# Performance work log

Hardware: AMD Instinct MI355X
Metric: run time of the kernel (lower is better)

Reference implementation:

```python
import jax, jax.numpy as jnp
import numpy as np

B, S, E, H = 2, 2048, 1024, 16
D = E // H  # head_dim = 64


def setup_inputs() -> dict:
    key = jax.random.key(0)
    ks = jax.random.split(key, 9)
    s = 1.0 / np.sqrt(E)
    return {
        "x": jax.random.normal(ks[0], (B, S, E), dtype=jnp.float32),
        "Wq": jax.random.uniform(ks[1], (E, E), jnp.float32, -s, s),
        "bq": jax.random.uniform(ks[2], (E,), jnp.float32, -s, s),
        "Wk": jax.random.uniform(ks[3], (E, E), jnp.float32, -s, s),
        "bk": jax.random.uniform(ks[4], (E,), jnp.float32, -s, s),
        "Wv": jax.random.uniform(ks[5], (E, E), jnp.float32, -s, s),
        "bv": jax.random.uniform(ks[6], (E,), jnp.float32, -s, s),
        "Wo": jax.random.uniform(ks[7], (E, E), jnp.float32, -s, s),
        "bo": jax.random.uniform(ks[8], (E,), jnp.float32, -s, s),
    }


def reference(x, Wq, bq, Wk, bk, Wv, bv, Wo, bo):
    # QKV projections (torch Linear: x @ W.T + b), split into heads: [B,H,S,D]
    def proj(t, W, b):
        return (t @ W.T + b).reshape(B, S, H, D).transpose(0, 2, 1, 3)

    Q = proj(x, Wq, bq)
    K = proj(x, Wk, bk)
    V = proj(x, Wv, bv)
    # scores [B,H,S,S], scaled by sqrt(head_dim)
    score = jnp.einsum('bnqd,bnkd->bnqk', Q, K) / jnp.sqrt(jnp.float32(D))
    weights = jax.nn.softmax(score, axis=-1)
    out = jnp.einsum('bnql,bnld->bnqd', weights, V)  # [B,H,S,D]
    out = out.transpose(0, 2, 1, 3).reshape(B, S, E)
    return out @ Wo.T + bo
```

## Files before the change

### kernel.cpp

```cpp
#include <hip/hip_runtime.h>


#define B_ 2
#define S_ 2048
#define E_ 1024
#define H_ 16
#define D_ 64
#define M_ (B_ * S_)

typedef __attribute__((ext_vector_type(8))) _Float16 f16x8;
typedef __attribute__((ext_vector_type(4))) _Float16 f16x4;
typedef __attribute__((ext_vector_type(2))) _Float16 f16x2;
typedef __attribute__((ext_vector_type(4))) float f32x4;
typedef __attribute__((ext_vector_type(16))) float f32x16;
typedef __attribute__((ext_vector_type(8))) unsigned short u16x8;
typedef __attribute__((ext_vector_type(4))) unsigned int u32x4;

#define LOG2E  1.44269504f
#define CLOG2  4.32808512f

#define KROW 144
#define KBUF 9216
#define VBASE 18432
#define SMEMSZ 36864

static __device__ __forceinline__ float bf16_to_f32(unsigned short u) {
    return __uint_as_float(((unsigned)u) << 16);
}
static __device__ __forceinline__ unsigned short f32_to_bf16(float f) {
    unsigned u = __float_as_uint(f);
    u += 0x7FFFu + ((u >> 16) & 1u);
    return (unsigned short)(u >> 16);
}
static __device__ __forceinline__ float load1_f32(const void* p, int i, bool isbf) {
    return isbf ? bf16_to_f32(((const unsigned short*)p)[i]) : ((const float*)p)[i];
}
static __device__ __forceinline__ void store1(void* p, size_t i, float v, bool isbf) {
    if (isbf) ((unsigned short*)p)[i] = f32_to_bf16(v);
    else      ((float*)p)[i] = v;
}
static __device__ __forceinline__ void gl2lds16(const void* g, void* l) {
    __builtin_amdgcn_global_load_lds((const __attribute__((address_space(1))) unsigned int*)g,
                                     (__attribute__((address_space(3))) unsigned int*)l, 16, 0, 0);
}
static __device__ __forceinline__ float rexp2(float x) {
    float r;
    asm("v_exp_f32 %0, %1" : "=v"(r) : "v"(x));
    return r;
}
static __device__ __forceinline__ unsigned pk2(float a, float b) {
    return __builtin_bit_cast(unsigned, __builtin_amdgcn_cvt_pkrtz(a, b));
}

__global__ __launch_bounds__(256) void convert_inputs(
    const void* __restrict__ x,  const void* __restrict__ wq,
    const void* __restrict__ wk, const void* __restrict__ wv,
    const void* __restrict__ wo,
    _Float16* __restrict__ x16, _Float16* __restrict__ w16,
    int* __restrict__ flag_out)
{
    __shared__ int sflag;
    const int tid = threadIdx.x;
    if (tid < 64) {
        const unsigned short hh = ((const unsigned short*)x)[2 * tid];
        const int e = (hh >> 7) & 0xFF;
        const bool sane = (e >= 0x60 && e <= 0x9F);
        const unsigned long long m = __ballot(sane);
        if (tid == 0) sflag = (__popcll(m) >= 48) ? 1 : 0;
    }
    __syncthreads();
    const bool isbf = sflag != 0;
    if (blockIdx.x == 0 && tid == 0) *flag_out = sflag;

    const size_t t = ((size_t)blockIdx.x * 256 + tid) * 8;
    const void* src; size_t off; _Float16* dst; float scale = 1.0f;
    if (t < (size_t)M_ * E_) { src = x; off = t; dst = x16 + t; }
    else {
        const size_t u = t - (size_t)M_ * E_;
        const int wsel = (int)(u >> 20);
        off = u & ((1u << 20) - 1);
        src = wsel == 0 ? wq : wsel == 1 ? wk : wsel == 2 ? wv : wo;
        dst = w16 + u;
        if (wsel == 0) scale = 0.125f * LOG2E;
    }
    f16x8 v;
    if (isbf) {
        u16x8 s = *(const u16x8*)((const unsigned short*)src + off);
        #pragma unroll
        for (int j = 0; j < 8; ++j) v[j] = (_Float16)(bf16_to_f32(s[j]) * scale);
    } else {
        const float* f = (const float*)src + off;
        f32x4 lo = *(const f32x4*)f;
        f32x4 hi = *(const f32x4*)(f + 4);
        #pragma unroll
        for (int j = 0; j < 4; ++j) {
            v[j]     = (_Float16)(lo[j] * scale);
            v[4 + j] = (_Float16)(hi[j] * scale);
        }
    }
    *(f16x8*)dst = v;
}

__global__ __launch_bounds__(256) void gemm_qkv(
    const _Float16* __restrict__ x16, const _Float16* __restrict__ w16,
    const void* __restrict__ bq, const void* __restrict__ bk, const void* __restrict__ bv,
    const int* __restrict__ flag,
    _Float16* __restrict__ Qb, _Float16* __restrict__ Kb, _Float16* __restrict__ VTb)
{
    __shared__ __align__(16) _Float16 As[128 * 64];
    __shared__ __align__(16) _Float16 Bs[128 * 64];
    const bool isbf = (*flag != 0);
    const int tid = threadIdx.x, wave = tid >> 6, lane = tid & 63;
    const int wm = wave >> 1, wn = wave & 1;
    const int qd = lane >> 4, ln = lane & 15;
    const int m0 = blockIdx.x * 128;
    const int by = blockIdx.y;
    const int wsel = by >> 3;
    const int n0 = (by & 7) * 128;
    const _Float16* W = w16 + ((size_t)wsel << 20);

    char* dX = (wsel == 2) ? (char*)Bs : (char*)As;
    char* dW = (wsel == 2) ? (char*)As : (char*)Bs;

    const _Float16* gx[4]; const _Float16* gw[4];
    char* lx[4]; char* lw[4];
    #pragma unroll
    for (int it = 0; it < 4; ++it) {
        const int seg = it * 256 + tid;
        const int row = seg >> 3, cg = seg & 7;
        const int scol = ((cg + row) & 7) * 8;
        gx[it] = x16 + (size_t)(m0 + row) * E_ + scol;
        gw[it] = W + (size_t)(n0 + row) * E_ + scol;
        lx[it] = dX + (size_t)(it * 256 + wave * 64) * 16;
        lw[it] = dW + (size_t)(it * 256 + wave * 64) * 16;
    }

    const int sw0 = ((qd - ln) & 7) * 8;
    const int sw1 = ((qd + 4 - ln) & 7) * 8;

    f32x4 acc[16] = {};

    for (int kt = 0; kt < E_; kt += 64) {
        __syncthreads();
        #pragma unroll
        for (int it = 0; it < 4; ++it) {
            gl2lds16(gx[it] + kt, lx[it]);
            gl2lds16(gw[it] + kt, lw[it]);
        }
        __syncthreads();
        #pragma unroll
        for (int kk = 0; kk < 2; ++kk) {
            const int sw = kk ? sw1 : sw0;
            f16x8 a[4], bfr[4];
            #pragma unroll
            for (int mt = 0; mt < 4; ++mt)
                a[mt] = *(const f16x8*)&As[((wm * 64 + mt * 16 + ln) << 6) + sw];
            #pragma unroll
            for (int nt = 0; nt < 4; ++nt)
                bfr[nt] = *(const f16x8*)&Bs[((wn * 64 + nt * 16 + ln) << 6) + sw];
            #pragma unroll
            for (int mt = 0; mt < 4; ++mt)
                #pragma unroll
                for (int nt = 0; nt < 4; ++nt)
                    acc[mt * 4 + nt] = __builtin_amdgcn_mfma_f32_16x16x32_f16(a[mt], bfr[nt], acc[mt * 4 + nt], 0, 0, 0);
        }
    }

    if (wsel != 2) {
        const void* bias = wsel == 0 ? bq : bk;
        const float bscale = (wsel == 0) ? 0.125f * LOG2E : 1.0f;
        _Float16* dst = wsel == 0 ? Qb : Kb;
        #pragma unroll
        for (int nt = 0; nt < 4; ++nt) {
            const int n = n0 + wn * 64 + nt * 16 + ln;
            const float bvv = load1_f32(bias, n, isbf) * bscale;
            const int h = n >> 6, d = n & 63;
            #pragma unroll
            for (int mt = 0; mt < 4; ++mt)
                #pragma unroll
                for (int r = 0; r < 4; ++r) {
                    const int m = m0 + wm * 64 + mt * 16 + qd * 4 + r;
                    const int b = m >> 11, s = m & (S_ - 1);
                    dst[((size_t)(b * H_ + h) * S_ + s) * D_ + d] =
                        (_Float16)(acc[mt * 4 + nt][r] + bvv);
                }
        }
    } else {
        #pragma unroll
        for (int mt = 0; mt < 4; ++mt)
            #pragma unroll
            for (int r = 0; r < 4; ++r) {
                const int e = n0 + wm * 64 + mt * 16 + qd * 4 + r;
                const float bvv = load1_f32(bv, e, isbf);
                const int h = e >> 6, d = e & 63;
                #pragma unroll
                for (int nt = 0; nt < 4; ++nt) {
                    const int sg = m0 + wn * 64 + nt * 16 + ln;
                    const int b = sg >> 11, s = sg & (S_ - 1);
                    VTb[((size_t)(b * H_ + h) * D_ + d) * S_ + s] =
                        (_Float16)(acc[mt * 4 + nt][r] + bvv);
                }
            }
    }
}

__global__ __launch_bounds__(256, 4) void attn(
    const _Float16* __restrict__ Q, const _Float16* __restrict__ K,
    const _Float16* __restrict__ VT, _Float16* __restrict__ AO)
{
    __shared__ __align__(16) char smem[SMEMSZ];

    const int tid = threadIdx.x, wave = tid >> 6, lane = tid & 63;
    const int rl = lane & 31, h = lane >> 5;
    const int qg = wave & 1, kh = wave >> 1;
    const int L = blockIdx.x;
    const int bh = ((L & 7) << 2) | ((L >> 3) & 3);
    const int qt = L >> 5;
    const int b = bh >> 4, hh = bh & (H_ - 1);

    const _Float16* Kbase = K + (size_t)bh * S_ * D_;
    const _Float16* Vbase = VT + (size_t)bh * D_ * S_;

    f16x8 qf[4];
    {
        const _Float16* qrow = Q + ((size_t)bh * S_ + qt * 64 + qg * 32 + rl) * D_ + h * 8;
        #pragma unroll
        for (int c = 0; c < 4; ++c) qf[c] = *(const f16x8*)(qrow + c * 16);
    }

    f16x8 ones;
    #pragma unroll
    for (int j = 0; j < 8; ++j) ones[j] = (_Float16)1.0f;

    const _Float16* kg[2]; const _Float16* vg[2]; int sw[2];
    #pragma unroll
    for (int it = 0; it < 2; ++it) {
        const int seg = it * 256 + tid;
        const int row = seg >> 3, c = seg & 7;
        kg[it] = Kbase + (size_t)row * D_ + c * 8;
        vg[it] = Vbase + (size_t)row * S_ + c * 8;
        sw[it] = row * KROW + c * 16;
    }

    int koff[4];
    #pragma unroll
    for (int c = 0; c < 4; ++c)
        koff[c] = (kh * 32 + rl) * KROW + (((c << 1) | h) << 4);
    const int vrow0 = rl * KROW, vrow1 = (32 + rl) * KROW;
    const int vka = kh * 64 + h * 8;

    f32x16 o0 = {}, o1 = {}, li = {};

    {
        f16x8 kr[2], vr[2];
        #pragma unroll
        for (int it = 0; it < 2; ++it) { kr[it] = *(const f16x8*)kg[it]; vr[it] = *(const f16x8*)vg[it]; }
        #pragma unroll
        for (int it = 0; it < 2; ++it) {
            *(f16x8*)(smem + sw[it])         = kr[it];
            *(f16x8*)(smem + VBASE + sw[it]) = vr[it];
        }
    }
    __syncthreads();

    for (int kt = 0; kt < S_; kt += 64) {
        const int p = (kt >> 6) & 1;
        const bool more = (kt + 64) < S_;

        f16x8 kr[2], vr[2];
        if (more) {
            #pragma unroll
            for (int it = 0; it < 2; ++it) {
                kr[it] = *(const f16x8*)(kg[it] + (size_t)(kt + 64) * D_);
                vr[it] = *(const f16x8*)(vg[it] + (kt + 64));
            }
        }

        const char* kb = smem + p * KBUF;
        const char* vb = smem + VBASE + p * KBUF;

        f16x8 af[4];
        #pragma unroll
        for (int c = 0; c < 4; ++c) af[c] = *(const f16x8*)(kb + koff[c]);

        f32x16 sc = {};
        __builtin_amdgcn_s_setprio(1);
        #pragma unroll
        for (int c = 0; c < 4; ++c)
            sc = __builtin_amdgcn_mfma_f32_32x32x16_f16(af[c], qf[c], sc, 0, 0, 0);
        __builtin_amdgcn_s_setprio(0);

        float e[16];
        #pragma unroll
        for (int i = 0; i < 16; ++i) e[i] = rexp2(sc[i] - CLOG2);

        #pragma unroll
        for (int ks = 0; ks < 2; ++ks) {
            const int oo = 8 * ks;
            const f16x8 pf = __builtin_bit_cast(f16x8, (u32x4){
                pk2(e[oo + 0], e[oo + 1]), pk2(e[oo + 2], e[oo + 3]),
                pk2(e[oo + 4], e[oo + 5]), pk2(e[oo + 6], e[oo + 7])});

            const int cA = vka + ks * 32;
            const f16x4 a0 = *(const f16x4*)(vb + vrow0 + cA);
            const f16x4 b0 = *(const f16x4*)(vb + vrow0 + cA + 16);
            const f16x4 a1 = *(const f16x4*)(vb + vrow1 + cA);
            const f16x4 b1 = *(const f16x4*)(vb + vrow1 + cA + 16);
            const f16x8 v0 = __builtin_shufflevector(a0, b0, 0, 1, 2, 3, 4, 5, 6, 7);
            const f16x8 v1 = __builtin_shufflevector(a1, b1, 0, 1, 2, 3, 4, 5, 6, 7);

            __builtin_amdgcn_s_setprio(1);
            o0 = __builtin_amdgcn_mfma_f32_32x32x16_f16(pf, v0, o0, 0, 0, 0);
            o1 = __builtin_amdgcn_mfma_f32_32x32x16_f16(pf, v1, o1, 0, 0, 0);
            li = __builtin_amdgcn_mfma_f32_32x32x16_f16(pf, ones, li, 0, 0, 0);
            __builtin_amdgcn_s_setprio(0);
        }

        if (more) {
            #pragma unroll
            for (int it = 0; it < 2; ++it) {
                *(f16x8*)(smem + (p ^ 1) * KBUF + sw[it])         = kr[it];
                *(f16x8*)(smem + VBASE + (p ^ 1) * KBUF + sw[it]) = vr[it];
            }
        }
        __syncthreads();
    }

    float* red = (float*)smem;
    const int rbase = qg * 64 + lane;
    if (kh) {
        #pragma unroll
        for (int i = 0; i < 16; ++i) {
            red[i * 128 + rbase]        = o0[i];
            red[(16 + i) * 128 + rbase] = o1[i];
            red[(32 + i) * 128 + rbase] = li[i];
        }
    }
    __syncthreads();
    if (!kh) {
        #pragma unroll
        for (int i = 0; i < 16; ++i) {
            const float t0 = o0[i] + red[i * 128 + rbase];
            const float t1 = o1[i] + red[(16 + i) * 128 + rbase];
            const float tl = li[i] + red[(32 + i) * 128 + rbase];
            const float inv = 1.0f / tl;
            const int q = qt * 64 + qg * 32 + 4 * h + (i & 3) + 8 * (i >> 2);
            _Float16* dst = AO + ((size_t)b * S_ + q) * E_ + hh * D_;
            dst[rl]      = (_Float16)(t0 * inv);
            dst[32 + rl] = (_Float16)(t1 * inv);
        }
    }
}

__global__ __launch_bounds__(256) void gemm_out(
    const _Float16* __restrict__ A, const _Float16* __restrict__ W,
    const void* __restrict__ bias, const int* __restrict__ flag, void* __restrict__ out)
{
    __shared__ __align__(16) _Float16 As[128 * 64];
    __shared__ __align__(16) _Float16 Bs[128 * 64];
    const bool isbf = (*flag != 0);
    const int tid = threadIdx.x, wave = tid >> 6, lane = tid & 63;
    const int wm = wave >> 1, wn = wave & 1;
    const int qd = lane >> 4, ln = lane & 15;
    const int m0 = blockIdx.x * 128;
    const int n0 = blockIdx.y * 128;

    const _Float16* ga[4]; const _Float16* gb[4];
    char* la[4]; char* lb[4];
    #pragma unroll
    for (int it = 0; it < 4; ++it) {
        const int seg = it * 256 + tid;
        const int row = seg >> 3, cg = seg & 7;
        const int scol = ((cg + row) & 7) * 8;
        ga[it] = A + (size_t)(m0 + row) * E_ + scol;
        gb[it] = W + (size_t)(n0 + row) * E_ + scol;
        la[it] = (char*)As + (size_t)(it * 256 + wave * 64) * 16;
        lb[it] = (char*)Bs + (size_t)(it * 256 + wave * 64) * 16;
    }
    const int sw0 = ((qd - ln) & 7) * 8;
    const int sw1 = ((qd + 4 - ln) & 7) * 8;

    f32x4 acc[16] = {};

    for (int kt = 0; kt < E_; kt += 64) {
        __syncthreads();
        #pragma unroll
        for (int it = 0; it < 4; ++it) {
            gl2lds16(ga[it] + kt, la[it]);
            gl2lds16(gb[it] + kt, lb[it]);
        }
        __syncthreads();
        #pragma unroll
        for (int kk = 0; kk < 2; ++kk) {
            const int sw = kk ? sw1 : sw0;
            f16x8 a[4], bfr[4];
            #pragma unroll
            for (int mt = 0; mt < 4; ++mt)
                a[mt] = *(const f16x8*)&As[((wm * 64 + mt * 16 + ln) << 6) + sw];
            #pragma unroll
            for (int nt = 0; nt < 4; ++nt)
                bfr[nt] = *(const f16x8*)&Bs[((wn * 64 + nt * 16 + ln) << 6) + sw];
            #pragma unroll
            for (int mt = 0; mt < 4; ++mt)
                #pragma unroll
                for (int nt = 0; nt < 4; ++nt)
                    acc[mt * 4 + nt] = __builtin_amdgcn_mfma_f32_16x16x32_f16(a[mt], bfr[nt], acc[mt * 4 + nt], 0, 0, 0);
        }
    }

    #pragma unroll
    for (int nt = 0; nt < 4; ++nt) {
        const int n = n0 + wn * 64 + nt * 16 + ln;
        const float bvv = load1_f32(bias, n, isbf);
        #pragma unroll
        for (int mt = 0; mt < 4; ++mt)
            #pragma unroll
            for (int r = 0; r < 4; ++r) {
                const int m = m0 + wm * 64 + mt * 16 + qd * 4 + r;
                store1(out, (size_t)m * E_ + n, acc[mt * 4 + nt][r] + bvv, isbf);
            }
    }
}

extern "C" void kernel_launch(void* const* d_in, const int* in_sizes, int n_in,
                              void* d_out, int out_size, void* d_ws, size_t ws_size,
                              hipStream_t stream) {
    const void* x  = d_in[0];
    const void* Wq = d_in[1];
    const void* bq = d_in[2];
    const void* Wk = d_in[3];
    const void* bk = d_in[4];
    const void* Wv = d_in[5];
    const void* bv = d_in[6];
    const void* Wo = d_in[7];
    const void* bo = d_in[8];

    int* flag = (int*)d_ws;
    _Float16* x16 = (_Float16*)((char*)d_ws + 1024);
    _Float16* w16 = x16 + (size_t)M_ * E_;
    _Float16* Qb  = w16 + 4u * (size_t)E_ * E_;
    _Float16* Kb  = Qb + (size_t)M_ * E_;
    _Float16* VTb = Kb + (size_t)M_ * E_;
    _Float16* AO  = x16;

    convert_inputs<<<4096, 256, 0, stream>>>(x, Wq, Wk, Wv, Wo, x16, w16, flag);
    gemm_qkv<<<dim3(32, 24), 256, 0, stream>>>(x16, w16, bq, bk, bv, flag, Qb, Kb, VTb);
    attn<<<1024, 256, 0, stream>>>(Qb, Kb, VTb, AO);
    gemm_out<<<dim3(32, 8), 256, 0, stream>>>(AO, w16 + 3u * (size_t)E_ * E_, bo, flag, d_out);
}
```

Measured before the change: 204.1 us.

## Replace ones-MFMA row sum with VALU sum and restructure K/V prefetch pipeline

```diff
diff --git a/kernel.cpp b/kernel.cpp
--- a/kernel.cpp
+++ b/kernel.cpp
@@ -228,10 +228,6 @@
         for (int c = 0; c < 4; ++c) qf[c] = *(const f16x8*)(qrow + c * 16);
     }
 
-    f16x8 ones;
-    #pragma unroll
-    for (int j = 0; j < 8; ++j) ones[j] = (_Float16)1.0f;
-
     const _Float16* kg[2]; const _Float16* vg[2]; int sw[2];
     #pragma unroll
     for (int it = 0; it < 2; ++it) {
@@ -249,91 +245,100 @@
     const int vrow0 = rl * KROW, vrow1 = (32 + rl) * KROW;
     const int vka = kh * 64 + h * 8;
 
-    f32x16 o0 = {}, o1 = {}, li = {};
-
-    {
-        f16x8 kr[2], vr[2];
-        #pragma unroll
-        for (int it = 0; it < 2; ++it) { kr[it] = *(const f16x8*)kg[it]; vr[it] = *(const f16x8*)vg[it]; }
-        #pragma unroll
-        for (int it = 0; it < 2; ++it) {
-            *(f16x8*)(smem + sw[it])         = kr[it];
-            *(f16x8*)(smem + VBASE + sw[it]) = vr[it];
-        }
+    f32x16 o0 = {}, o1 = {};
+    float lisum = 0.0f;
+
+    f16x8 kA[2], vA[2], kB[2], vB[2];
+
+    #pragma unroll
+    for (int it = 0; it < 2; ++it) { kA[it] = *(const f16x8*)kg[it]; vA[it] = *(const f16x8*)vg[it]; }
+    #pragma unroll
+    for (int it = 0; it < 2; ++it) {
+        *(f16x8*)(smem + sw[it])         = kA[it];
+        *(f16x8*)(smem + VBASE + sw[it]) = vA[it];
+    }
+    #pragma unroll
+    for (int it = 0; it < 2; ++it) {
+        kB[it] = *(const f16x8*)(kg[it] + (size_t)64 * D_);
+        vB[it] = *(const f16x8*)(vg[it] + 64);
     }
     __syncthreads();
 
-    for (int kt = 0; kt < S_; kt += 64) {
-        const int p = (kt >> 6) & 1;
-        const bool more = (kt + 64) < S_;
-
-        f16x8 kr[2], vr[2];
-        if (more) {
-            #pragma unroll
-            for (int it = 0; it < 2; ++it) {
-                kr[it] = *(const f16x8*)(kg[it] + (size_t)(kt + 64) * D_);
-                vr[it] = *(const f16x8*)(vg[it] + (kt + 64));
-            }
-        }
-
-        const char* kb = smem + p * KBUF;
-        const char* vb = smem + VBASE + p * KBUF;
-
-        f16x8 af[4];
-        #pragma unroll
-        for (int c = 0; c < 4; ++c) af[c] = *(const f16x8*)(kb + koff[c]);
-
-        f32x16 sc = {};
-        __builtin_amdgcn_s_setprio(1);
-        #pragma unroll
-        for (int c = 0; c < 4; ++c)
-            sc = __builtin_amdgcn_mfma_f32_32x32x16_f16(af[c], qf[c], sc, 0, 0, 0);
-        __builtin_amdgcn_s_setprio(0);
-
-        float e[16];
-        #pragma unroll
-        for (int i = 0; i < 16; ++i) e[i] = rexp2(sc[i] - CLOG2);
-
-        #pragma unroll
-        for (int ks = 0; ks < 2; ++ks) {
-            const int oo = 8 * ks;
-            const f16x8 pf = __builtin_bit_cast(f16x8, (u32x4){
-                pk2(e[oo + 0], e[oo + 1]), pk2(e[oo + 2], e[oo + 3]),
-                pk2(e[oo + 4], e[oo + 5]), pk2(e[oo + 6], e[oo + 7])});
-
-            const int cA = vka + ks * 32;
-            const f16x4 a0 = *(const f16x4*)(vb + vrow0 + cA);
-            const f16x4 b0 = *(const f16x4*)(vb + vrow0 + cA + 16);
-            const f16x4 a1 = *(const f16x4*)(vb + vrow1 + cA);
-            const f16x4 b1 = *(const f16x4*)(vb + vrow1 + cA + 16);
-            const f16x8 v0 = __builtin_shufflevector(a0, b0, 0, 1, 2, 3, 4, 5, 6, 7);
-            const f16x8 v1 = __builtin_shufflevector(a1, b1, 0, 1, 2, 3, 4, 5, 6, 7);
-
-            __builtin_amdgcn_s_setprio(1);
-            o0 = __builtin_amdgcn_mfma_f32_32x32x16_f16(pf, v0, o0, 0, 0, 0);
-            o1 = __builtin_amdgcn_mfma_f32_32x32x16_f16(pf, v1, o1, 0, 0, 0);
-            li = __builtin_amdgcn_mfma_f32_32x32x16_f16(pf, ones, li, 0, 0, 0);
-            __builtin_amdgcn_s_setprio(0);
-        }
-
-        if (more) {
-            #pragma unroll
-            for (int it = 0; it < 2; ++it) {
-                *(f16x8*)(smem + (p ^ 1) * KBUF + sw[it])         = kr[it];
-                *(f16x8*)(smem + VBASE + (p ^ 1) * KBUF + sw[it]) = vr[it];
-            }
-        }
-        __syncthreads();
-    }
+    #define ISSUE(t, kr, vr)                                              \
+        { _Pragma("unroll")                                               \
+          for (int it = 0; it < 2; ++it) {                                \
+              kr[it] = *(const f16x8*)(kg[it] + (size_t)(t) * 64 * D_);   \
+              vr[it] = *(const f16x8*)(vg[it] + (t) * 64);                \
+          } }
+    #define LWRITE(pb, kr, vr)                                            \
+        { _Pragma("unroll")                                               \
+          for (int it = 0; it < 2; ++it) {                                \
+              *(f16x8*)(smem + (pb) * KBUF + sw[it])         = kr[it];    \
+              *(f16x8*)(smem + VBASE + (pb) * KBUF + sw[it]) = vr[it];    \
+          } }
+
+    #define COMPUTE(pb)                                                          \
+    {                                                                            \
+        const char* kb = smem + (pb) * KBUF;                                     \
+        const char* vb = smem + VBASE + (pb) * KBUF;                             \
+        f16x8 af[4];                                                             \
+        _Pragma("unroll")                                                        \
+        for (int c = 0; c < 4; ++c) af[c] = *(const f16x8*)(kb + koff[c]);       \
+        f32x16 sc = {};                                                          \
+        __builtin_amdgcn_s_setprio(1);                                           \
+        _Pragma("unroll")                                                        \
+        for (int c = 0; c < 4; ++c)                                              \
+            sc = __builtin_amdgcn_mfma_f32_32x32x16_f16(af[c], qf[c], sc, 0, 0, 0); \
+        __builtin_amdgcn_s_setprio(0);                                           \
+        float e[16];                                                             \
+        _Pragma("unroll")                                                        \
+        for (int i = 0; i < 16; ++i) e[i] = rexp2(sc[i] - CLOG2);                \
+        lisum += (((e[0] + e[1]) + (e[2] + e[3])) + ((e[4] + e[5]) + (e[6] + e[7])))   \
+               + (((e[8] + e[9]) + (e[10] + e[11])) + ((e[12] + e[13]) + (e[14] + e[15]))); \
+        _Pragma("unroll")                                                        \
+        for (int ks = 0; ks < 2; ++ks) {                                         \
+            const int oo = 8 * ks;                                               \
+            const f16x8 pf = __builtin_bit_cast(f16x8, (u32x4){                  \
+                pk2(e[oo + 0], e[oo + 1]), pk2(e[oo + 2], e[oo + 3]),            \
+                pk2(e[oo + 4], e[oo + 5]), pk2(e[oo + 6], e[oo + 7])});          \
+            const int cA = vka + ks * 32;                                        \
+            const f16x4 a0 = *(const f16x4*)(vb + vrow0 + cA);                   \
+            const f16x4 b0 = *(const f16x4*)(vb + vrow0 + cA + 16);              \
+            const f16x4 a1 = *(const f16x4*)(vb + vrow1 + cA);                   \
+            const f16x4 b1 = *(const f16x4*)(vb + vrow1 + cA + 16);              \
+            const f16x8 v0 = __builtin_shufflevector(a0, b0, 0, 1, 2, 3, 4, 5, 6, 7); \
+            const f16x8 v1 = __builtin_shufflevector(a1, b1, 0, 1, 2, 3, 4, 5, 6, 7); \
+            __builtin_amdgcn_s_setprio(1);                                       \
+            o0 = __builtin_amdgcn_mfma_f32_32x32x16_f16(pf, v0, o0, 0, 0, 0);    \
+            o1 = __builtin_amdgcn_mfma_f32_32x32x16_f16(pf, v1, o1, 0, 0, 0);    \
+            __builtin_amdgcn_s_setprio(0);                                       \
+        }                                                                        \
+    }
+
+    for (int t = 0; t < 32; t += 2) {
+        if (t + 2 < 32) ISSUE(t + 2, kA, vA);
+        COMPUTE(0);
+        LWRITE(1, kB, vB);
+        __syncthreads();
+        if (t + 3 < 32) ISSUE(t + 3, kB, vB);
+        COMPUTE(1);
+        if (t + 2 < 32) LWRITE(0, kA, vA);
+        __syncthreads();
+    }
+
+    #undef ISSUE
+    #undef LWRITE
+    #undef COMPUTE
 
     float* red = (float*)smem;
+    float* lig = (float*)(smem + 16384);
     const int rbase = qg * 64 + lane;
+    lig[(qg * 32 + rl) * 4 + kh * 2 + h] = lisum;
     if (kh) {
         #pragma unroll
         for (int i = 0; i < 16; ++i) {
             red[i * 128 + rbase]        = o0[i];
             red[(16 + i) * 128 + rbase] = o1[i];
-            red[(32 + i) * 128 + rbase] = li[i];
         }
     }
     __syncthreads();
@@ -342,9 +347,10 @@
         for (int i = 0; i < 16; ++i) {
             const float t0 = o0[i] + red[i * 128 + rbase];
             const float t1 = o1[i] + red[(16 + i) * 128 + rbase];
-            const float tl = li[i] + red[(32 + i) * 128 + rbase];
-            const float inv = 1.0f / tl;
-            const int q = qt * 64 + qg * 32 + 4 * h + (i & 3) + 8 * (i >> 2);
+            const int ql = qg * 32 + 4 * h + (i & 3) + 8 * (i >> 2);
+            const f32x4 lv = *(const f32x4*)&lig[ql * 4];
+            const float inv = 1.0f / ((lv[0] + lv[1]) + (lv[2] + lv[3]));
+            const int q = qt * 64 + ql;
             _Float16* dst = AO + ((size_t)b * S_ + q) * E_ + hh * D_;
             dst[rl]      = (_Float16)(t0 * inv);
             dst[32 + rl] = (_Float16)(t1 * inv);
```

New measurement: 239.0 us. 17.1% more time.
